# Kernel optimization log

Measured on AMD Instinct MI355X. Metric: run time of the kernel, lower is better.

Reference implementation:

```python
import jax, jax.numpy as jnp
import numpy as np

B, P, C, F = 16, 1000, 91, 1024      # images, proposals/img, classes (incl bg), box-head dim
H, W = 800, 800                      # image shape (all images same size)
SCORE_THRESH = 0.05
NMS_THRESH = 0.5
DETS = 100                           # detections_per_img
MIN_SIZE = 1e-2
BBOX_XFORM_CLIP = float(np.log(1000.0 / 16.0))
OFF = float(max(H, W) + 2)           # class offset unit for batched (class-aware) NMS


def setup_inputs() -> dict:
    key = jax.random.key(0)
    k1, k2, k3, k4 = jax.random.split(key, 4)
    box_features = jax.random.normal(k1, (B * P, F), jnp.float32)
    Wc = jax.random.normal(k2, (F, C), jnp.float32) * 0.02
    bc = jnp.zeros((C,), jnp.float32)
    Wb = jax.random.normal(k3, (F, C * 4), jnp.float32) * 0.02
    bb = jnp.zeros((C * 4,), jnp.float32)
    u = jax.random.uniform(k4, (B, P, 4), jnp.float32)
    x1 = u[..., 0] * (W * 0.8)
    y1 = u[..., 1] * (H * 0.8)
    x2 = x1 + 16.0 + u[..., 2] * (W * 0.2)
    y2 = y1 + 16.0 + u[..., 3] * (H * 0.2)
    proposals = jnp.stack([x1, y1, x2, y2], axis=-1)
    return dict(box_features=box_features, Wc=Wc, bc=bc, Wb=Wb, bb=bb,
                proposals=proposals)


def _decode_and_clip(regs, props):
    # regs: [N, C, 4] deltas; props: [N, 4] xyxy. bbox_reg_weights = (1,1,1,1).
    w = props[:, 2] - props[:, 0]
    h = props[:, 3] - props[:, 1]
    cx = props[:, 0] + 0.5 * w
    cy = props[:, 1] + 0.5 * h
    dx, dy = regs[..., 0], regs[..., 1]
    dw = jnp.minimum(regs[..., 2], BBOX_XFORM_CLIP)
    dh = jnp.minimum(regs[..., 3], BBOX_XFORM_CLIP)
    pcx = dx * w[:, None] + cx[:, None]
    pcy = dy * h[:, None] + cy[:, None]
    pw = jnp.exp(dw) * w[:, None]
    ph = jnp.exp(dh) * h[:, None]
    x1 = jnp.clip(pcx - 0.5 * pw, 0.0, float(W))
    y1 = jnp.clip(pcy - 0.5 * ph, 0.0, float(H))
    x2 = jnp.clip(pcx + 0.5 * pw, 0.0, float(W))
    y2 = jnp.clip(pcy + 0.5 * ph, 0.0, float(H))
    return jnp.stack([x1, y1, x2, y2], axis=-1)  # [N, C, 4]


def _iou_one_vs_all(box, boxes):
    ix1 = jnp.maximum(box[0], boxes[:, 0])
    iy1 = jnp.maximum(box[1], boxes[:, 1])
    ix2 = jnp.minimum(box[2], boxes[:, 2])
    iy2 = jnp.minimum(box[3], boxes[:, 3])
    inter = jnp.clip(ix2 - ix1, 0.0) * jnp.clip(iy2 - iy1, 0.0)
    a1 = (box[2] - box[0]) * (box[3] - box[1])
    a2 = (boxes[:, 2] - boxes[:, 0]) * (boxes[:, 3] - boxes[:, 1])
    return inter / (a1 + a2 - inter + 1e-9)


def _greedy_nms(boxes, scores):
    # boxes: [M,4] (class-offset), scores: [M] (-inf = filtered out).
    # Returns selected indices [DETS] and scores [DETS] (0 where no valid pick).
    def body(i, st):
        sc, sel, ss = st
        j = jnp.argmax(sc)
        s = sc[j]
        iou = _iou_one_vs_all(boxes[j], boxes)
        sc = jnp.where(iou > NMS_THRESH, -jnp.inf, sc)  # suppresses j itself too
        valid = s > 0.0
        sel = sel.at[i].set(jnp.where(valid, j.astype(jnp.int32), 0))
        ss = ss.at[i].set(jnp.where(valid, s, 0.0))
        return sc, sel, ss
    init = (scores, jnp.zeros((DETS,), jnp.int32), jnp.zeros((DETS,), jnp.float32))
    _, sel, ss = jax.lax.fori_loop(0, DETS, body, init)
    return sel, ss


def reference(box_features, Wc, bc, Wb, bb, proposals):
    # Box predictor (FastRCNNPredictor-style linear heads).
    class_logits = box_features @ Wc + bc                  # [B*P, C]
    box_regression = (box_features @ Wb + bb).reshape(-1, C, 4)
    # Decode per-class boxes against proposals, clip to image.
    pred = _decode_and_clip(box_regression, proposals.reshape(-1, 4))  # [B*P, C, 4]
    scores = jax.nn.softmax(class_logits, axis=-1)         # [B*P, C]
    # Drop background class 0; flatten (proposal, class) per image.
    M = P * (C - 1)
    boxes_all = pred[:, 1:, :].reshape(B, M, 4)
    scores_all = scores[:, 1:].reshape(B, M)
    labels_all = jnp.tile(jnp.arange(1, C, dtype=jnp.int32), P)  # [M]
    # Score threshold + remove tiny boxes (mask instead of dynamic filter).
    bw = boxes_all[..., 2] - boxes_all[..., 0]
    bh = boxes_all[..., 3] - boxes_all[..., 1]
    keep = (scores_all > SCORE_THRESH) & (bw >= MIN_SIZE) & (bh >= MIN_SIZE)
    scores_m = jnp.where(keep, scores_all, -jnp.inf)
    # Class-aware batched NMS via per-class coordinate offsets.
    boxes_off = boxes_all + (labels_all.astype(jnp.float32) * OFF)[None, :, None]
    sel, det_scores = jax.vmap(_greedy_nms)(boxes_off, scores_m)   # [B,DETS]
    det_boxes = jnp.take_along_axis(boxes_all, sel[..., None], axis=1)  # [B,DETS,4]
    det_labels = labels_all[sel]                                        # [B,DETS]
    valid = det_scores > 0.0
    det_boxes = det_boxes * valid[..., None]
    det_labels = jnp.where(valid, det_labels, 0)
    return det_boxes, det_scores, det_labels
```

## Files before the change

kernel.cpp:

```cpp
#include <hip/hip_runtime.h>
#include <hip/hip_bf16.h>
#include <math.h>

typedef unsigned long long ull;

#define BB_ 16
#define PP_ 1000
#define CC_ 91
#define FF_ 1024
#define DETS_ 100
#define CAP_ 2048
#define CAND_MAX (BB_ * CAP_)
#define SURV_CAP 2048
#define CLS_CAP 256
#define IMG_W 800.0f
#define IMG_H 800.0f
#define OFF_ 802.0f
#define SCORE_TH 0.05f
#define NMS_TH 0.5f
#define MIN_SZ 0.01f
#define BBOX_CLIP_D 4.135166556742356

__global__ __launch_bounds__(256) void logits_cand(
    const float* __restrict__ A, const float* __restrict__ Wc,
    const float* __restrict__ bc,
    float* __restrict__ cs, int* __restrict__ clab,
    int* __restrict__ corig, int* __restrict__ cpidx,
    int* __restrict__ cnt)
{
    __shared__ union SM {
        struct { double Ad[16][34]; double Bd[16][98]; } t;
        float Ssc[32][97];
    } sm;

    const int tid = threadIdx.x;
    const int row0 = blockIdx.x * 32;
    const int tx = tid & 31;
    const int ty = tid >> 5;
    const int tx3 = tx * 3, ty4 = ty * 4;

    const int am = tid >> 2;
    const int ak = (tid & 3) * 4;
    const int bk = tid >> 4;
    const int bn = (tid & 15) * 6;

    double acc[4][3];
#pragma unroll
    for (int i = 0; i < 4; ++i)
#pragma unroll
        for (int j = 0; j < 3; ++j) acc[i][j] = 0.0;

    float4 avP = make_float4(0.f, 0.f, 0.f, 0.f);
    if (tid < 128)
        avP = *reinterpret_cast<const float4*>(A + (size_t)(row0 + am) * FF_ + ak);
    float bvP[6];
#pragma unroll
    for (int jj = 0; jj < 6; ++jj) {
        const int c = bn + jj;
        bvP[jj] = (c < CC_) ? Wc[(size_t)bk * CC_ + c] : 0.f;
    }

    for (int k0 = 0; k0 < FF_; k0 += 16) {
        if (tid < 128) {
            sm.t.Ad[ak + 0][am] = (double)avP.x;
            sm.t.Ad[ak + 1][am] = (double)avP.y;
            sm.t.Ad[ak + 2][am] = (double)avP.z;
            sm.t.Ad[ak + 3][am] = (double)avP.w;
        }
#pragma unroll
        for (int jj = 0; jj < 6; ++jj) sm.t.Bd[bk][bn + jj] = (double)bvP[jj];

        const int kn = k0 + 16;
        if (kn < FF_) {
            if (tid < 128)
                avP = *reinterpret_cast<const float4*>(
                    A + (size_t)(row0 + am) * FF_ + kn + ak);
#pragma unroll
            for (int jj = 0; jj < 6; ++jj) {
                const int c = bn + jj;
                bvP[jj] = (c < CC_) ? Wc[(size_t)(kn + bk) * CC_ + c] : 0.f;
            }
        }
        __syncthreads();

#pragma unroll
        for (int k = 0; k < 16; ++k) {
            const double a0 = sm.t.Ad[k][ty4 + 0];
            const double a1 = sm.t.Ad[k][ty4 + 1];
            const double a2 = sm.t.Ad[k][ty4 + 2];
            const double a3 = sm.t.Ad[k][ty4 + 3];
            const double b0 = sm.t.Bd[k][tx3 + 0];
            const double b1 = sm.t.Bd[k][tx3 + 1];
            const double b2 = sm.t.Bd[k][tx3 + 2];
            acc[0][0] += a0 * b0; acc[0][1] += a0 * b1; acc[0][2] += a0 * b2;
            acc[1][0] += a1 * b0; acc[1][1] += a1 * b1; acc[1][2] += a1 * b2;
            acc[2][0] += a2 * b0; acc[2][1] += a2 * b1; acc[2][2] += a2 * b2;
            acc[3][0] += a3 * b0; acc[3][1] += a3 * b1; acc[3][2] += a3 * b2;
        }
        __syncthreads();
    }

#pragma unroll
    for (int i = 0; i < 4; ++i)
#pragma unroll
        for (int j = 0; j < 3; ++j) {
            const int c = tx3 + j;
            if (c < CC_) {
                const float lf = (float)acc[i][j];
                sm.Ssc[ty4 + i][c] = __fadd_rn(lf, bc[c]);
            }
        }
    __syncthreads();

    if (tid < 32) {
        const int p = row0 + tid;
        const int b = p / PP_;
        const int pi = p - b * PP_;

        float m = sm.Ssc[tid][0];
        for (int c = 1; c < CC_; ++c) m = fmaxf(m, sm.Ssc[tid][c]);
        double denom = 0.0;
        for (int c = 0; c < CC_; ++c)
            denom += exp((double)sm.Ssc[tid][c] - (double)m);

        for (int c = 1; c < CC_; ++c) {
            const double sd = exp((double)sm.Ssc[tid][c] - (double)m) / denom;
            const float score = (float)sd;
            if (score > SCORE_TH) {
                const int pos = atomicAdd(&cnt[b], 1);
                if (pos < CAP_) {
                    const int g = b * CAP_ + pos;
                    cs[g] = score;
                    clab[g] = c;
                    corig[g] = pi * (CC_ - 1) + (c - 1);
                    cpidx[g] = p;
                }
            }
        }
    }
}

__global__ __launch_bounds__(256) void decode_cand(
    const float* __restrict__ A, const float* __restrict__ Wb,
    const float* __restrict__ bb, const float* __restrict__ props,
    const int* __restrict__ cnt, const int* __restrict__ clab,
    const int* __restrict__ cpidx,
    float* __restrict__ cs, float* __restrict__ cx1, float* __restrict__ cy1,
    float* __restrict__ cx2, float* __restrict__ cy2)
{
    const int wid = (blockIdx.x * 256 + threadIdx.x) >> 6;
    const int lane = threadIdx.x & 63;
    const int b = wid / CAP_;
    const int pos = wid - b * CAP_;
    if (b >= BB_) return;
    const int n = min(cnt[b], CAP_);
    if (pos >= n) return;

    const int g = b * CAP_ + pos;
    const int p = cpidx[g];
    const int c = clab[g];

    const float* fr = A + (size_t)p * FF_;
    const float* wb0 = Wb + 4 * c;

    double a0 = 0.0, a1 = 0.0, a2 = 0.0, a3 = 0.0;
    for (int k = lane; k < FF_; k += 64) {
        const double f = (double)fr[k];
        const float4 wv = *reinterpret_cast<const float4*>(wb0 + (size_t)k * (CC_ * 4));
        a0 += f * (double)wv.x; a1 += f * (double)wv.y;
        a2 += f * (double)wv.z; a3 += f * (double)wv.w;
    }
#pragma unroll
    for (int off = 32; off > 0; off >>= 1) {
        a0 += __shfl_xor(a0, off);
        a1 += __shfl_xor(a1, off);
        a2 += __shfl_xor(a2, off);
        a3 += __shfl_xor(a3, off);
    }

    if (lane == 0) {
        const float dx = __fadd_rn((float)a0, bb[4 * c + 0]);
        const float dy = __fadd_rn((float)a1, bb[4 * c + 1]);
        const float clipf = (float)BBOX_CLIP_D;
        const float dw = fminf(__fadd_rn((float)a2, bb[4 * c + 2]), clipf);
        const float dh = fminf(__fadd_rn((float)a3, bb[4 * c + 3]), clipf);

        const float px1 = props[(size_t)p * 4 + 0];
        const float py1 = props[(size_t)p * 4 + 1];
        const float px2 = props[(size_t)p * 4 + 2];
        const float py2 = props[(size_t)p * 4 + 3];
        const float w = __fsub_rn(px2, px1);
        const float h = __fsub_rn(py2, py1);
        const float cx = __fadd_rn(px1, __fmul_rn(0.5f, w));
        const float cy = __fadd_rn(py1, __fmul_rn(0.5f, h));

        const float pcx = __fadd_rn(__fmul_rn(dx, w), cx);
        const float pcy = __fadd_rn(__fmul_rn(dy, h), cy);
        const float ew = (float)exp((double)dw);
        const float eh = (float)exp((double)dh);
        const float pw = __fmul_rn(ew, w);
        const float ph = __fmul_rn(eh, h);

        const float hw = __fmul_rn(0.5f, pw);
        const float hh = __fmul_rn(0.5f, ph);
        const float bx1 = fminf(fmaxf(__fsub_rn(pcx, hw), 0.f), IMG_W);
        const float by1 = fminf(fmaxf(__fsub_rn(pcy, hh), 0.f), IMG_H);
        const float bx2 = fminf(fmaxf(__fadd_rn(pcx, hw), 0.f), IMG_W);
        const float by2 = fminf(fmaxf(__fadd_rn(pcy, hh), 0.f), IMG_H);

        cx1[g] = bx1; cy1[g] = by1; cx2[g] = bx2; cy2[g] = by2;
        if (!(__fsub_rn(bx2, bx1) >= MIN_SZ && __fsub_rn(by2, by1) >= MIN_SZ)) {
            cs[g] = -INFINITY;
        }
    }
}

__global__ __launch_bounds__(64) void nms_class(
    const float* __restrict__ c_x1, const float* __restrict__ c_y1,
    const float* __restrict__ c_x2, const float* __restrict__ c_y2,
    const float* __restrict__ c_s, const int* __restrict__ c_lab,
    const int* __restrict__ c_orig, const int* __restrict__ cnt,
    ull* __restrict__ skey, float* __restrict__ sx1v, float* __restrict__ sy1v,
    float* __restrict__ sx2v, float* __restrict__ sy2v,
    int* __restrict__ slabv, int* __restrict__ scnt)
{
    const int blk = blockIdx.x;
    const int b = blk / (CC_ - 1);
    const int c = 1 + (blk - b * (CC_ - 1));
    const int lane = threadIdx.x;

    __shared__ ull kk[CLS_CAP];
    __shared__ float x1s[CLS_CAP], y1s[CLS_CAP], x2s[CLS_CAP], y2s[CLS_CAP];

    const int n = min(cnt[b], CAP_);

    int mcnt = 0;
    for (int i0 = 0; i0 < n; i0 += 64) {
        const int i = i0 + lane;
        bool take = false;
        float s = 0.f; int so = 0; int g = 0;
        if (i < n) {
            g = b * CAP_ + i;
            if (c_lab[g] == c) {
                s = c_s[g];
                if (s > 0.f) { take = true; so = c_orig[g]; }
            }
        }
        const ull bal = __ballot(take);
        if (take) {
            const int pos = mcnt + __popcll(bal & ((1ull << lane) - 1ull));
            if (pos < CLS_CAP) {
                kk[pos] = ((ull)__float_as_uint(s) << 32) |
                          (unsigned int)(0x7FFFFFFF - so);
                x1s[pos] = c_x1[g]; y1s[pos] = c_y1[g];
                x2s[pos] = c_x2[g]; y2s[pos] = c_y2[g];
            }
        }
        mcnt += (int)__popcll(bal);
    }
    mcnt = min(mcnt, CLS_CAP);
    if (mcnt == 0) return;
    __syncthreads();

    while (true) {
        ull best = 0ull;
        for (int i = lane; i < mcnt; i += 64) best = (kk[i] > best) ? kk[i] : best;
#pragma unroll
        for (int off = 32; off > 0; off >>= 1) {
            const ull o = __shfl_xor(best, off);
            best = (o > best) ? o : best;
        }
        if (best == 0ull) break;

        int wsl = -1;
        for (int i = lane; i < mcnt; i += 64) if (kk[i] == best) wsl = i;
        const ull bal = __ballot(wsl >= 0);
        const int wlane = (int)__ffsll((long long)bal) - 1;
        wsl = __shfl(wsl, wlane);

        const float wx1 = x1s[wsl], wy1 = y1s[wsl];
        const float wx2 = x2s[wsl], wy2 = y2s[wsl];

        if (lane == 0) {
            const int sp = atomicAdd(&scnt[b], 1);
            if (sp < SURV_CAP) {
                const int sg = b * SURV_CAP + sp;
                skey[sg] = best;
                sx1v[sg] = wx1; sy1v[sg] = wy1;
                sx2v[sg] = wx2; sy2v[sg] = wy2;
                slabv[sg] = c;
            }
        }

        const float off = __fmul_rn((float)c, OFF_);
        const float ax1 = __fadd_rn(wx1, off), ay1 = __fadd_rn(wy1, off);
        const float ax2 = __fadd_rn(wx2, off), ay2 = __fadd_rn(wy2, off);
        const float a1 = __fmul_rn(__fsub_rn(ax2, ax1), __fsub_rn(ay2, ay1));
        for (int i = lane; i < mcnt; i += 64) {
            if (kk[i] == 0ull) continue;
            const float bx1 = __fadd_rn(x1s[i], off), by1 = __fadd_rn(y1s[i], off);
            const float bx2 = __fadd_rn(x2s[i], off), by2 = __fadd_rn(y2s[i], off);
            const float ix1 = fmaxf(ax1, bx1), iy1 = fmaxf(ay1, by1);
            const float ix2 = fminf(ax2, bx2), iy2 = fminf(ay2, by2);
            const float inter = __fmul_rn(fmaxf(__fsub_rn(ix2, ix1), 0.f),
                                          fmaxf(__fsub_rn(iy2, iy1), 0.f));
            const float a2 = __fmul_rn(__fsub_rn(bx2, bx1), __fsub_rn(by2, by1));
            const float den = __fadd_rn(__fsub_rn(__fadd_rn(a1, a2), inter), 1e-9f);
            const float iou = __fdiv_rn(inter, den);
            if (iou > NMS_TH) kk[i] = 0ull;
        }
        __syncthreads();
    }
}

__global__ __launch_bounds__(256) void nms_merge(
    const ull* __restrict__ skey, const float* __restrict__ sx1v,
    const float* __restrict__ sy1v, const float* __restrict__ sx2v,
    const float* __restrict__ sy2v, const int* __restrict__ slabv,
    const int* __restrict__ scnt, float* __restrict__ out)
{
    const int b = blockIdx.x;
    const int t = threadIdx.x;

    __shared__ ull k_[SURV_CAP];
    __shared__ int id_[SURV_CAP];

    const int m = min(scnt[b], SURV_CAP);
    int N2 = 128;
    while (N2 < m) N2 <<= 1;

    for (int i = t; i < N2; i += 256) {
        k_[i] = (i < m) ? skey[b * SURV_CAP + i] : 0ull;
        id_[i] = i;
    }
    __syncthreads();

    for (int ksz = 2; ksz <= N2; ksz <<= 1) {
        for (int j = ksz >> 1; j > 0; j >>= 1) {
            for (int i = t; i < N2; i += 256) {
                const int ixj = i ^ j;
                if (ixj > i) {
                    const ull a = k_[i], cc = k_[ixj];
                    const bool desc = ((i & ksz) == 0);
                    if (desc ? (a < cc) : (a > cc)) {
                        k_[i] = cc; k_[ixj] = a;
                        const int tmp = id_[i]; id_[i] = id_[ixj]; id_[ixj] = tmp;
                    }
                }
            }
            __syncthreads();
        }
    }

    const int boxes_base = 0;
    const int scores_base = BB_ * DETS_ * 4;
    const int labels_base = BB_ * DETS_ * 5;

    for (int r = t; r < DETS_; r += 256) {
        const ull key = (r < N2) ? k_[r] : 0ull;
        float* bo = out + boxes_base + (size_t)(b * DETS_ + r) * 4;
        if (key != 0ull) {
            const int sg = b * SURV_CAP + id_[r];
            bo[0] = sx1v[sg]; bo[1] = sy1v[sg];
            bo[2] = sx2v[sg]; bo[3] = sy2v[sg];
            out[scores_base + b * DETS_ + r] = __uint_as_float((unsigned)(key >> 32));
            out[labels_base + b * DETS_ + r] = (float)slabv[sg];
        } else {
            bo[0] = 0.f; bo[1] = 0.f; bo[2] = 0.f; bo[3] = 0.f;
            out[scores_base + b * DETS_ + r] = 0.f;
            out[labels_base + b * DETS_ + r] = 0.f;
        }
    }
}

extern "C" void kernel_launch(void* const* d_in, const int* in_sizes, int n_in,
                              void* d_out, int out_size, void* d_ws, size_t ws_size,
                              hipStream_t stream)
{
    const float* feat  = (const float*)d_in[0];
    const float* Wc    = (const float*)d_in[1];
    const float* bc    = (const float*)d_in[2];
    const float* Wb    = (const float*)d_in[3];
    const float* bb    = (const float*)d_in[4];
    const float* props = (const float*)d_in[5];
    for (int i = 0; i < n_in; ++i) {
        const float* q = (const float*)d_in[i];
        switch (in_sizes[i]) {
            case 16384000: feat  = q; break;
            case 93184:    Wc    = q; break;
            case 91:       bc    = q; break;
            case 372736:   Wb    = q; break;
            case 364:      bb    = q; break;
            case 64000:    props = q; break;
        }
    }
    float* out = (float*)d_out;

    char* ws = (char*)d_ws;
    int*   cnt   = (int*)ws;
    int*   scnt  = (int*)(ws + 64);
    float* cs    = (float*)(ws + 256);
    int*   clab  = (int*)(cs + CAND_MAX);
    int*   corig = clab + CAND_MAX;
    int*   cpidx = corig + CAND_MAX;
    float* cx1   = (float*)(cpidx + CAND_MAX);
    float* cy1   = cx1 + CAND_MAX;
    float* cx2   = cy1 + CAND_MAX;
    float* cy2   = cx2 + CAND_MAX;
    ull*   skey  = (ull*)(cy2 + CAND_MAX);
    float* sx1v  = (float*)(skey + (size_t)BB_ * SURV_CAP);
    float* sy1v  = sx1v + (size_t)BB_ * SURV_CAP;
    float* sx2v  = sy1v + (size_t)BB_ * SURV_CAP;
    float* sy2v  = sx2v + (size_t)BB_ * SURV_CAP;
    int*   slabv = (int*)(sy2v + (size_t)BB_ * SURV_CAP);

    hipMemsetAsync(ws, 0, 256, stream);

    logits_cand<<<500, 256, 0, stream>>>(feat, Wc, bc,
        cs, clab, corig, cpidx, cnt);

    decode_cand<<<CAND_MAX / 4, 256, 0, stream>>>(feat, Wb, bb, props,
        cnt, clab, cpidx, cs, cx1, cy1, cx2, cy2);

    nms_class<<<BB_ * (CC_ - 1), 64, 0, stream>>>(
        cx1, cy1, cx2, cy2, cs, clab, corig, cnt,
        skey, sx1v, sy1v, sx2v, sy2v, slabv, scnt);

    nms_merge<<<BB_, 256, 0, stream>>>(
        skey, sx1v, sy1v, sx2v, sy2v, slabv, scnt, out);
}
```

Before: 295.8 us.

## Pre-convert Wc to padded double and retile logits GEMM to 16-row blocks

A new small kernel converts the classifier weights to a padded 96-column double array once per call, so the logits kernel loads doubles with vector double2 reads instead of converting scalar floats every tile. The logits kernel is retiled to 16 rows per block with 128 threads and a 2x6 per-thread micro-tile, and A is kept in shared memory as float, converted to double on read. Blocks go from 500 to 1000 to raise occupancy and parallelism. The cost is an extra launch, extra workspace for the double weights, and double the weight traffic per block row.

```diff
diff --git a/kernel.cpp b/kernel.cpp
--- a/kernel.cpp
+++ b/kernel.cpp
@@ -21,98 +21,100 @@
 #define MIN_SZ 0.01f
 #define BBOX_CLIP_D 4.135166556742356
 
-__global__ __launch_bounds__(256) void logits_cand(
-    const float* __restrict__ A, const float* __restrict__ Wc,
+__global__ __launch_bounds__(256) void wc_to_double(
+    const float* __restrict__ Wc, double* __restrict__ Wcd)
+{
+    const int idx = blockIdx.x * 256 + threadIdx.x;
+    if (idx >= FF_ * 96) return;
+    const int k = idx / 96, c = idx - k * 96;
+    Wcd[idx] = (c < CC_) ? (double)Wc[(size_t)k * CC_ + c] : 0.0;
+}
+
+__global__ __launch_bounds__(128) void logits_cand(
+    const float* __restrict__ A, const double* __restrict__ Wcd,
     const float* __restrict__ bc,
     float* __restrict__ cs, int* __restrict__ clab,
     int* __restrict__ corig, int* __restrict__ cpidx,
     int* __restrict__ cnt)
 {
-    __shared__ union SM {
-        struct { double Ad[16][34]; double Bd[16][98]; } t;
-        float Ssc[32][97];
+    __shared__ union __align__(16) SM {
+        struct { double Bd[16][98]; float Af[16][18]; } t;
+        float Ssc[16][97];
     } sm;
 
     const int tid = threadIdx.x;
-    const int row0 = blockIdx.x * 32;
-    const int tx = tid & 31;
-    const int ty = tid >> 5;
-    const int tx3 = tx * 3, ty4 = ty * 4;
-
-    const int am = tid >> 2;
-    const int ak = (tid & 3) * 4;
-    const int bk = tid >> 4;
-    const int bn = (tid & 15) * 6;
-
-    double acc[4][3];
-#pragma unroll
-    for (int i = 0; i < 4; ++i)
-#pragma unroll
-        for (int j = 0; j < 3; ++j) acc[i][j] = 0.0;
-
-    float4 avP = make_float4(0.f, 0.f, 0.f, 0.f);
-    if (tid < 128)
-        avP = *reinterpret_cast<const float4*>(A + (size_t)(row0 + am) * FF_ + ak);
-    float bvP[6];
-#pragma unroll
-    for (int jj = 0; jj < 6; ++jj) {
-        const int c = bn + jj;
-        bvP[jj] = (c < CC_) ? Wc[(size_t)bk * CC_ + c] : 0.f;
-    }
+    const int row0 = blockIdx.x * 16;
+
+    const int ty2 = (tid >> 4) * 2;
+    const int tx6 = (tid & 15) * 6;
+
+    const int ar  = tid >> 3;
+    const int ak2 = (tid & 7) * 2;
+    const int bk  = tid >> 3;
+    const int bco = (tid & 7) * 12;
+
+    double acc[2][6];
+#pragma unroll
+    for (int i = 0; i < 2; ++i)
+#pragma unroll
+        for (int j = 0; j < 6; ++j) acc[i][j] = 0.0;
+
+    float2 avP = *reinterpret_cast<const float2*>(
+        A + (size_t)(row0 + ar) * FF_ + ak2);
+    double2 bvP[6];
+#pragma unroll
+    for (int j = 0; j < 6; ++j)
+        bvP[j] = *reinterpret_cast<const double2*>(
+            Wcd + (size_t)bk * 96 + bco + 2 * j);
 
     for (int k0 = 0; k0 < FF_; k0 += 16) {
-        if (tid < 128) {
-            sm.t.Ad[ak + 0][am] = (double)avP.x;
-            sm.t.Ad[ak + 1][am] = (double)avP.y;
-            sm.t.Ad[ak + 2][am] = (double)avP.z;
-            sm.t.Ad[ak + 3][am] = (double)avP.w;
-        }
-#pragma unroll
-        for (int jj = 0; jj < 6; ++jj) sm.t.Bd[bk][bn + jj] = (double)bvP[jj];
+        sm.t.Af[ak2 + 0][ar] = avP.x;
+        sm.t.Af[ak2 + 1][ar] = avP.y;
+#pragma unroll
+        for (int j = 0; j < 6; ++j)
+            *reinterpret_cast<double2*>(&sm.t.Bd[bk][bco + 2 * j]) = bvP[j];
 
         const int kn = k0 + 16;
         if (kn < FF_) {
-            if (tid < 128)
-                avP = *reinterpret_cast<const float4*>(
-                    A + (size_t)(row0 + am) * FF_ + kn + ak);
-#pragma unroll
-            for (int jj = 0; jj < 6; ++jj) {
-                const int c = bn + jj;
-                bvP[jj] = (c < CC_) ? Wc[(size_t)(kn + bk) * CC_ + c] : 0.f;
-            }
+            avP = *reinterpret_cast<const float2*>(
+                A + (size_t)(row0 + ar) * FF_ + kn + ak2);
+#pragma unroll
+            for (int j = 0; j < 6; ++j)
+                bvP[j] = *reinterpret_cast<const double2*>(
+                    Wcd + (size_t)(kn + bk) * 96 + bco + 2 * j);
         }
         __syncthreads();
 
 #pragma unroll
         for (int k = 0; k < 16; ++k) {
-            const double a0 = sm.t.Ad[k][ty4 + 0];
-            const double a1 = sm.t.Ad[k][ty4 + 1];
-            const double a2 = sm.t.Ad[k][ty4 + 2];
-            const double a3 = sm.t.Ad[k][ty4 + 3];
-            const double b0 = sm.t.Bd[k][tx3 + 0];
-            const double b1 = sm.t.Bd[k][tx3 + 1];
-            const double b2 = sm.t.Bd[k][tx3 + 2];
-            acc[0][0] += a0 * b0; acc[0][1] += a0 * b1; acc[0][2] += a0 * b2;
-            acc[1][0] += a1 * b0; acc[1][1] += a1 * b1; acc[1][2] += a1 * b2;
-            acc[2][0] += a2 * b0; acc[2][1] += a2 * b1; acc[2][2] += a2 * b2;
-            acc[3][0] += a3 * b0; acc[3][1] += a3 * b1; acc[3][2] += a3 * b2;
+            const float2 af = *reinterpret_cast<const float2*>(&sm.t.Af[k][ty2]);
+            const double a0 = (double)af.x, a1 = (double)af.y;
+            const double2 b01 = *reinterpret_cast<const double2*>(&sm.t.Bd[k][tx6 + 0]);
+            const double2 b23 = *reinterpret_cast<const double2*>(&sm.t.Bd[k][tx6 + 2]);
+            const double2 b45 = *reinterpret_cast<const double2*>(&sm.t.Bd[k][tx6 + 4]);
+            acc[0][0] += a0 * b01.x; acc[0][1] += a0 * b01.y;
+            acc[0][2] += a0 * b23.x; acc[0][3] += a0 * b23.y;
+            acc[0][4] += a0 * b45.x; acc[0][5] += a0 * b45.y;
+            acc[1][0] += a1 * b01.x; acc[1][1] += a1 * b01.y;
+            acc[1][2] += a1 * b23.x; acc[1][3] += a1 * b23.y;
+            acc[1][4] += a1 * b45.x; acc[1][5] += a1 * b45.y;
         }
         __syncthreads();
     }
 
 #pragma unroll
-    for (int i = 0; i < 4; ++i)
-#pragma unroll
-        for (int j = 0; j < 3; ++j) {
-            const int c = tx3 + j;
+    for (int i = 0; i < 2; ++i)
+#pragma unroll
+        for (int j = 0; j < 6; ++j) {
+            const int c = tx6 + j;
             if (c < CC_) {
                 const float lf = (float)acc[i][j];
-                sm.Ssc[ty4 + i][c] = __fadd_rn(lf, bc[c]);
+                sm.Ssc[ty2 + i][c] = __fadd_rn(lf, bc[c]);
             }
         }
     __syncthreads();
 
-    if (tid < 32) {
+    if (tid < 16) {
         const int p = row0 + tid;
         const int b = p / PP_;
         const int pi = p - b * PP_;
@@ -413,10 +415,13 @@
     float* sx2v  = sy1v + (size_t)BB_ * SURV_CAP;
     float* sy2v  = sx2v + (size_t)BB_ * SURV_CAP;
     int*   slabv = (int*)(sy2v + (size_t)BB_ * SURV_CAP);
+    double* Wcd  = (double*)(slabv + (size_t)BB_ * SURV_CAP);
 
     hipMemsetAsync(ws, 0, 256, stream);
 
-    logits_cand<<<500, 256, 0, stream>>>(feat, Wc, bc,
+    wc_to_double<<<(FF_ * 96 + 255) / 256, 256, 0, stream>>>(Wc, Wcd);
+
+    logits_cand<<<PP_ * BB_ / 16, 128, 0, stream>>>(feat, Wcd, bc,
         cs, clab, corig, cpidx, cnt);
 
     decode_cand<<<CAND_MAX / 4, 256, 0, stream>>>(feat, Wb, bb, props,
```

Result: slower. 391.5 us (+32.4%).
